# Performance work log

Hardware: AMD Instinct MI355X
Metric: run time of the kernel (lower is better)

The kernel has to match this reference:

```python
import jax, jax.numpy as jnp
import numpy as np

B, L, D = 16, 2048, 1024  # memory_len == input_len (mask is applied on both axes)
NEG = -1e20


def setup_inputs() -> dict:
    key = jax.random.key(0)
    k1, k2, k3, k4, k5, k6 = jax.random.split(key, 6)
    inp = jax.random.normal(k1, (B, L, D), dtype=jnp.float32)
    mem = jax.random.normal(k2, (B, L, D), dtype=jnp.float32)
    # True = masked-out position; keep sparsity low so rows stay mostly valid
    mask = jax.random.bernoulli(k3, 0.1, (B, L))
    inv = 1.0 / np.sqrt(D)
    w_input = jax.random.normal(k4, (D,), dtype=jnp.float32) * inv   # Linear(D,1) weight
    w_memory = jax.random.normal(k5, (D,), dtype=jnp.float32) * inv  # Linear(D,1) weight
    dot_scale = jax.random.uniform(k6, (D,), dtype=jnp.float32, minval=0.0, maxval=inv)
    return {"input": inp, "memory": mem, "mask": mask,
            "w_input": w_input, "w_memory": w_memory, "dot_scale": dot_scale}


def reference(input, memory, mask, w_input, w_memory, dot_scale):
    # dropout p = 0.0 -> identity
    input_dot = jnp.einsum("bld,d->bl", input, w_input)[:, :, None]   # [B,L,1]
    memory_dot = jnp.einsum("bmd,d->bm", memory, w_memory)[:, None, :]  # [B,1,M]
    cross_dot = jnp.einsum("bld,bmd->blm", input * dot_scale, memory)   # [B,L,M]
    att = input_dot + memory_dot + cross_dot
    bad = mask[:, :, None] | mask[:, None, :]                           # [B,L,M]
    att = jnp.where(bad, NEG, att)
    weight_one = jax.nn.softmax(att, axis=-1)                           # over memory axis
    output_one = jnp.einsum("blm,bmd->bld", weight_one, memory)
    weight_two = jax.nn.softmax(att.max(axis=-1), axis=-1)[:, None, :]  # [B,1,L]
    output_two = jnp.einsum("bol,bld->bod", weight_two, input)          # [B,1,D]
    return jnp.concatenate(
        [input, output_one, input * output_one, output_two * output_one], axis=-1)
```

## Files before the change

### kernel.cpp

```cpp
#include <hip/hip_runtime.h>
#include <hip/hip_bf16.h>


#define BDIM 16
#define LDIM 2048
#define MDIM 2048
#define DDIM 1024
#define NEGF (-60000.0f)

typedef float    f32x4v __attribute__((ext_vector_type(4)));
typedef _Float16 half8  __attribute__((ext_vector_type(8)));
typedef _Float16 half4  __attribute__((ext_vector_type(4)));

#define GL16(gp, lp)                                                        \
  __builtin_amdgcn_global_load_lds(                                         \
      (const __attribute__((address_space(1))) unsigned int*)(gp),          \
      (__attribute__((address_space(3))) unsigned int*)(lp), 16, 0, 0)

__device__ __forceinline__ float4 m4(const float4 a, const float4 b) {
  return (float4){a.x * b.x, a.y * b.y, a.z * b.z, a.w * b.w};
}
__device__ __forceinline__ void nts4(const float4 v, float* p) {
  f32x4v w = {v.x, v.y, v.z, v.w};
  __builtin_nontemporal_store(w, (f32x4v*)p);
}

__global__ __launch_bounds__(256) void conv_kernel(
    const float* __restrict__ input, const float* __restrict__ memory,
    const float* __restrict__ w_in, const float* __restrict__ w_mem,
    const float* __restrict__ scale,
    _Float16* __restrict__ Qh, _Float16* __restrict__ Kh,
    float* __restrict__ idot, float* __restrict__ mdot) {
  const int t = threadIdx.x, lane = t & 63, wid = t >> 6;
  const size_t row = (size_t)blockIdx.x * 4 + wid;
  const float* ir  = input  + row * DDIM;
  const float* mrp = memory + row * DDIM;
  float di = 0.f, dm = 0.f;
#pragma unroll
  for (int c = 0; c < 4; ++c) {
    const int off = c * 256 + lane * 4;
    float4 sc4 = *(const float4*)&scale[off];
    float4 wi4 = *(const float4*)&w_in[off];
    float4 wm4 = *(const float4*)&w_mem[off];
    float4 v = *(const float4*)&ir[off];
    di += v.x * wi4.x + v.y * wi4.y + v.z * wi4.z + v.w * wi4.w;
    half4 q = { (_Float16)(v.x * sc4.x), (_Float16)(v.y * sc4.y),
                (_Float16)(v.z * sc4.z), (_Float16)(v.w * sc4.w) };
    *(half4*)&Qh[row * DDIM + off] = q;
    float4 u = *(const float4*)&mrp[off];
    dm += u.x * wm4.x + u.y * wm4.y + u.z * wm4.z + u.w * wm4.w;
    half4 k = { (_Float16)u.x, (_Float16)u.y, (_Float16)u.z, (_Float16)u.w };
    *(half4*)&Kh[row * DDIM + off] = k;
  }
#pragma unroll
  for (int o = 1; o < 64; o <<= 1) {
    di += __shfl_xor(di, o, 64);
    dm += __shfl_xor(dm, o, 64);
  }
  if (lane == 0) { idot[row] = di; mdot[row] = dm; }
}

__global__ __launch_bounds__(256) void tr_kernel(const _Float16* __restrict__ Kh,
                                                 _Float16* __restrict__ Vt) {
  const int b = blockIdx.z;
  const int d0 = blockIdx.x * 64, m0 = blockIdx.y * 64;
  __shared__ _Float16 sT[64][80];
  const int t = threadIdx.x;
  {
    const int mr = t >> 2, ch = (t & 3) * 16;
    const _Float16* src = Kh + ((size_t)b * MDIM + m0 + mr) * DDIM + d0 + ch;
    *(half8*)&sT[mr][ch]     = *(const half8*)&src[0];
    *(half8*)&sT[mr][ch + 8] = *(const half8*)&src[8];
  }
  __syncthreads();
  {
    const int dr = t >> 2, mc = (t & 3) * 16;
    union { _Float16 h[16]; half8 v[2]; } tmp;
#pragma unroll
    for (int j = 0; j < 16; ++j) tmp.h[j] = sT[mc + j][dr];
    _Float16* dst = Vt + ((size_t)b * DDIM + d0 + dr) * MDIM + m0 + mc;
    *(half8*)&dst[0] = tmp.v[0];
    *(half8*)&dst[8] = tmp.v[1];
  }
}

__device__ __forceinline__ void stage128(const _Float16* __restrict__ Ab,
                                         const _Float16* __restrict__ Bb,
                                         _Float16* sAb, _Float16* sBb,
                                         int stride, int k0, int wid, int lane) {
  const int rsub = lane >> 3;
  const int sc = ((lane & 7) ^ rsub) * 8;
#pragma unroll
  for (int j = 0; j < 4; ++j) {
    const int r0 = wid * 32 + j * 8;
    const size_t go = (size_t)(r0 + rsub) * stride + k0 + sc;
    GL16(Ab + go, sAb + r0 * 64);
    GL16(Bb + go, sBb + r0 * 64);
  }
}

__device__ __forceinline__ void compute128(const _Float16* sAb, const _Float16* sBb,
                                           f32x4v acc[4][4], int wr, int wc,
                                           int lane) {
  const int l15 = lane & 15;
#pragma unroll
  for (int kk = 0; kk < 2; ++kk) {
    const int colh = ((kk * 4 + (lane >> 4)) ^ (lane & 7)) * 8;
    half8 aF[4], bF[4];
#pragma unroll
    for (int i = 0; i < 4; ++i) {
      aF[i] = *(const half8*)&sAb[(wr * 64 + i * 16 + l15) * 64 + colh];
      bF[i] = *(const half8*)&sBb[(wc * 64 + i * 16 + l15) * 64 + colh];
    }
#pragma unroll
    for (int mi = 0; mi < 4; ++mi)
#pragma unroll
      for (int ni = 0; ni < 4; ++ni)
        acc[mi][ni] = __builtin_amdgcn_mfma_f32_16x16x32_f16(aF[mi], bF[ni],
                                                             acc[mi][ni], 0, 0, 0);
  }
}

__global__ __launch_bounds__(256, 4) void gemm1_kernel(
    const _Float16* __restrict__ Qh, const _Float16* __restrict__ Kh,
    const float* __restrict__ idot, const float* __restrict__ mdot,
    const int* __restrict__ mask, _Float16* __restrict__ Sp) {
  const int id = blockIdx.x;
  const int wg = (id & 7) * 512 + (id >> 3);
  const int b = wg >> 8, rem = wg & 255, by = rem >> 4, bx = rem & 15;
  const int t = threadIdx.x, lane = t & 63, wid = t >> 6;
  const int wr = wid >> 1, wc = wid & 1;
  __shared__ union SM1 {
    struct { _Float16 a[128 * 64]; _Float16 b[128 * 64]; } ab;
    _Float16 s[128 * 140];
  } sm;
  __shared__ float s_dl[128], s_dm[128];
  __shared__ int   s_ml[128], s_mm[128];
  if (t < 128) {
    s_dl[t] = idot[b * LDIM + by * 128 + t];
    s_ml[t] = mask[b * LDIM + by * 128 + t];
    s_dm[t] = mdot[b * MDIM + bx * 128 + t];
    s_mm[t] = mask[b * MDIM + bx * 128 + t];
  }
  const _Float16* Ab = Qh + ((size_t)b * LDIM + by * 128) * DDIM;
  const _Float16* Bb = Kh + ((size_t)b * MDIM + bx * 128) * DDIM;
  f32x4v acc[4][4];
#pragma unroll
  for (int i = 0; i < 4; ++i)
#pragma unroll
    for (int j = 0; j < 4; ++j) acc[i][j] = (f32x4v){0.f, 0.f, 0.f, 0.f};

  for (int ks = 0; ks < DDIM / 64; ++ks) {
    __syncthreads();
    stage128(Ab, Bb, sm.ab.a, sm.ab.b, DDIM, ks * 64, wid, lane);
    __syncthreads();
    compute128(sm.ab.a, sm.ab.b, acc, wr, wc, lane);
  }

  __syncthreads();
  const int rb = wr * 64, cb = wc * 64;
#pragma unroll
  for (int mi = 0; mi < 4; ++mi)
#pragma unroll
    for (int ni = 0; ni < 4; ++ni)
#pragma unroll
      for (int r = 0; r < 4; ++r) {
        const int lrow = rb + mi * 16 + (lane >> 4) * 4 + r;
        const int lcol = cb + ni * 16 + (lane & 15);
        float s = acc[mi][ni][r] + s_dl[lrow] + s_dm[lcol];
        if ((s_ml[lrow] | s_mm[lcol]) != 0) s = NEGF;
        sm.s[lrow * 140 + lcol] = (_Float16)s;
      }
  __syncthreads();
  const int r16 = t >> 4, c8 = (t & 15) * 8;
#pragma unroll
  for (int rd = 0; rd < 8; ++rd) {
    const int lrow = rd * 16 + r16;
    half8 v = *(const half8*)&sm.s[lrow * 140 + c8];
    *(half8*)&Sp[((size_t)b * LDIM + by * 128 + lrow) * MDIM + bx * 128 + c8] = v;
  }
}

__global__ __launch_bounds__(256) void softmax_rows(_Float16* __restrict__ Sp,
                                                    float* __restrict__ rmax) {
  const int t = threadIdx.x, lane = t & 63, wid = t >> 6;
  const size_t row = (size_t)blockIdx.x * 4 + wid;
  _Float16* rp = Sp + row * (size_t)MDIM;
  float s[32];
#pragma unroll
  for (int c = 0; c < 4; ++c) {
    half8 v = *(const half8*)&rp[c * 512 + lane * 8];
#pragma unroll
    for (int j = 0; j < 8; ++j) s[c * 8 + j] = (float)v[j];
  }
  float m = -3.0e38f;
#pragma unroll
  for (int i = 0; i < 32; ++i) m = fmaxf(m, s[i]);
#pragma unroll
  for (int o = 1; o < 64; o <<= 1) m = fmaxf(m, __shfl_xor(m, o, 64));
  float sum = 0.f;
#pragma unroll
  for (int i = 0; i < 32; ++i) { s[i] = __expf(s[i] - m); sum += s[i]; }
#pragma unroll
  for (int o = 1; o < 64; o <<= 1) sum += __shfl_xor(sum, o, 64);
  const float inv = 1.f / sum;
#pragma unroll
  for (int c = 0; c < 4; ++c) {
    half8 v;
#pragma unroll
    for (int j = 0; j < 8; ++j) v[j] = (_Float16)(s[c * 8 + j] * inv);
    *(half8*)&rp[c * 512 + lane * 8] = v;
  }
  if (lane == 0) rmax[row] = m;
}

__global__ __launch_bounds__(256) void w2a_kernel(const float* __restrict__ rmax,
                                                  float* __restrict__ w2,
                                                  float* __restrict__ o2) {
  const int b = blockIdx.x, t = threadIdx.x;
  ((float4*)(o2 + (size_t)b * DDIM))[t] = (float4){0.f, 0.f, 0.f, 0.f};
  __shared__ float red[256];
  const float* rm = rmax + (size_t)b * LDIM;
  float vals[8]; float lm = -3.0e38f;
#pragma unroll
  for (int j = 0; j < 8; ++j) { vals[j] = rm[t + j * 256]; lm = fmaxf(lm, vals[j]); }
  red[t] = lm; __syncthreads();
  for (int s = 128; s > 0; s >>= 1) {
    if (t < s) red[t] = fmaxf(red[t], red[t + s]);
    __syncthreads();
  }
  const float M = red[0]; __syncthreads();
  float ls = 0.f;
#pragma unroll
  for (int j = 0; j < 8; ++j) ls += __expf(vals[j] - M);
  red[t] = ls; __syncthreads();
  for (int s = 128; s > 0; s >>= 1) {
    if (t < s) red[t] += red[t + s];
    __syncthreads();
  }
  const float inv = 1.f / red[0];
#pragma unroll
  for (int j = 0; j < 8; ++j) w2[(size_t)b * LDIM + t + j * 256] = __expf(vals[j] - M) * inv;
}

__global__ __launch_bounds__(256) void o2_kernel(const float* __restrict__ input,
                                                 const float* __restrict__ w2,
                                                 float* __restrict__ o2) {
  const int b = blockIdx.y, ch = blockIdx.x, t = threadIdx.x;
  __shared__ float sw[128];
  if (t < 128) sw[t] = w2[(size_t)b * LDIM + ch * 128 + t];
  __syncthreads();
  const float* ib = input + ((size_t)b * LDIM + ch * 128) * DDIM;
  float4 acc = {0.f, 0.f, 0.f, 0.f};
  for (int l = 0; l < 128; ++l) {
    const float w = sw[l];
    float4 v = *(const float4*)&ib[(size_t)l * DDIM + t * 4];
    acc.x += w * v.x; acc.y += w * v.y; acc.z += w * v.z; acc.w += w * v.w;
  }
  atomicAdd(&o2[b * DDIM + t * 4 + 0], acc.x);
  atomicAdd(&o2[b * DDIM + t * 4 + 1], acc.y);
  atomicAdd(&o2[b * DDIM + t * 4 + 2], acc.z);
  atomicAdd(&o2[b * DDIM + t * 4 + 3], acc.w);
}

__global__ __launch_bounds__(256, 4) void gemm2_kernel(
    const _Float16* __restrict__ Pm, const _Float16* __restrict__ Vt,
    const float* __restrict__ input, const float* __restrict__ o2,
    float* __restrict__ out) {
  const int id = blockIdx.x;
  const int wg = (id & 7) * 256 + (id >> 3);
  const int b = wg >> 7, rem = wg & 127, by = rem >> 3, bx = rem & 7;
  const int t = threadIdx.x, lane = t & 63, wid = t >> 6;
  const int wr = wid >> 1, wc = wid & 1;
  __shared__ union SM2 {
    struct { _Float16 a[128 * 64]; _Float16 b[128 * 64]; } ab;
    float c[16 * 132];
  } sm;
  const _Float16* Ab = Pm + ((size_t)b * LDIM + by * 128) * MDIM;
  const _Float16* Bb = Vt + ((size_t)b * DDIM + bx * 128) * MDIM;
  f32x4v acc[4][4];
#pragma unroll
  for (int i = 0; i < 4; ++i)
#pragma unroll
    for (int j = 0; j < 4; ++j) acc[i][j] = (f32x4v){0.f, 0.f, 0.f, 0.f};

  for (int ks = 0; ks < MDIM / 64; ++ks) {
    __syncthreads();
    stage128(Ab, Bb, sm.ab.a, sm.ab.b, MDIM, ks * 64, wid, lane);
    __syncthreads();
    compute128(sm.ab.a, sm.ab.b, acc, wr, wc, lane);
  }

  const int cq = (t & 15) * 4;
  const float4 o2a = *(const float4*)&o2[b * DDIM + bx * 128 + cq];
  const float4 o2b = *(const float4*)&o2[b * DDIM + bx * 128 + 64 + cq];
  const int r16 = t >> 4;
  __syncthreads();
#pragma unroll
  for (int pp = 0; pp < 8; ++pp) {
    if (wr == (pp >> 2)) {
      const int pmi = pp & 3;
#pragma unroll
      for (int ni = 0; ni < 4; ++ni)
#pragma unroll
        for (int r = 0; r < 4; ++r)
          sm.c[((lane >> 4) * 4 + r) * 132 + wc * 64 + ni * 16 + (lane & 15)] =
              acc[pmi][ni][r];
    }
    __syncthreads();
    const size_t l = (size_t)by * 128 + pp * 16 + r16;
    const float4 c0 = *(const float4*)&sm.c[r16 * 132 + cq];
    const float4 c1 = *(const float4*)&sm.c[r16 * 132 + 64 + cq];
    const float* ibp = &input[((size_t)b * LDIM + l) * DDIM + bx * 128];
    const float4 i0 = *(const float4*)&ibp[cq];
    const float4 i1 = *(const float4*)&ibp[64 + cq];
    float* ob = &out[((size_t)b * LDIM + l) * (4 * DDIM) + bx * 128];
    nts4(i0, ob + cq);
    nts4(i1, ob + 64 + cq);
    nts4(c0, ob + DDIM + cq);
    nts4(c1, ob + DDIM + 64 + cq);
    nts4(m4(i0, c0), ob + 2 * DDIM + cq);
    nts4(m4(i1, c1), ob + 2 * DDIM + 64 + cq);
    nts4(m4(o2a, c0), ob + 3 * DDIM + cq);
    nts4(m4(o2b, c1), ob + 3 * DDIM + 64 + cq);
    __syncthreads();
  }
}

extern "C" void kernel_launch(void* const* d_in, const int* in_sizes, int n_in,
                              void* d_out, int out_size, void* d_ws, size_t ws_size,
                              hipStream_t stream) {
  (void)in_sizes; (void)n_in; (void)out_size; (void)ws_size;
  const float* input  = (const float*)d_in[0];
  const float* memory = (const float*)d_in[1];
  const int*   mask   = (const int*)d_in[2];
  const float* w_in   = (const float*)d_in[3];
  const float* w_mem  = (const float*)d_in[4];
  const float* scale  = (const float*)d_in[5];
  float* out = (float*)d_out;

  char* p = (char*)d_ws;
  _Float16* Qh = (_Float16*)p; p += (size_t)BDIM * LDIM * DDIM * 2;
  _Float16* Kh = (_Float16*)p; p += (size_t)BDIM * MDIM * DDIM * 2;
  _Float16* Vt = (_Float16*)p; p += (size_t)BDIM * DDIM * MDIM * 2;
  _Float16* Sp = (_Float16*)p; p += (size_t)BDIM * LDIM * MDIM * 2;
  float* idot = (float*)p; p += (size_t)BDIM * LDIM * 4;
  float* mdot = (float*)p; p += (size_t)BDIM * MDIM * 4;
  float* rmax = (float*)p; p += (size_t)BDIM * LDIM * 4;
  float* w2   = (float*)p; p += (size_t)BDIM * LDIM * 4;
  float* o2   = (float*)p; p += (size_t)BDIM * DDIM * 4;

  conv_kernel<<<dim3(BDIM * LDIM / 4), dim3(256), 0, stream>>>(
      input, memory, w_in, w_mem, scale, Qh, Kh, idot, mdot);
  tr_kernel<<<dim3(DDIM / 64, MDIM / 64, BDIM), dim3(256), 0, stream>>>(Kh, Vt);
  gemm1_kernel<<<dim3(BDIM * 16 * 16), dim3(256), 0, stream>>>(
      Qh, Kh, idot, mdot, mask, Sp);
  softmax_rows<<<dim3(BDIM * LDIM / 4), dim3(256), 0, stream>>>(Sp, rmax);
  w2a_kernel<<<dim3(BDIM), dim3(256), 0, stream>>>(rmax, w2, o2);
  o2_kernel<<<dim3(LDIM / 128, BDIM), dim3(256), 0, stream>>>(input, w2, o2);
  gemm2_kernel<<<dim3(BDIM * 16 * 8), dim3(256), 0, stream>>>(
      Sp, Vt, input, o2, out);
}
```

Baseline: 552.9 us.

## Fuse memory conversion with V transpose and split input conversion kernel

The memory-side fp16 conversion, the w_mem dot product and the K→V transpose are merged into one kernel. It writes Kh and the transposed Vt straight from registers through shared memory, so the separate transpose pass no longer re-reads Kh. The input-side conversion becomes its own kernel. The o2 reduction also uses smaller chunks (32 rows instead of 128), giving 4x more blocks and more parallelism at the cost of more atomics. The fused memory kernel launches only 512 blocks and loops over 16 d-chunks with two barriers each, which may limit occupancy.

```diff
diff --git a/kernel.cpp b/kernel.cpp
--- a/kernel.cpp
+++ b/kernel.cpp
@@ -25,63 +25,79 @@
   __builtin_nontemporal_store(w, (f32x4v*)p);
 }
 
-__global__ __launch_bounds__(256) void conv_kernel(
-    const float* __restrict__ input, const float* __restrict__ memory,
-    const float* __restrict__ w_in, const float* __restrict__ w_mem,
-    const float* __restrict__ scale,
-    _Float16* __restrict__ Qh, _Float16* __restrict__ Kh,
-    float* __restrict__ idot, float* __restrict__ mdot) {
+__global__ __launch_bounds__(256) void conv_in(
+    const float* __restrict__ input, const float* __restrict__ w_in,
+    const float* __restrict__ scale, _Float16* __restrict__ Qh,
+    float* __restrict__ idot) {
   const int t = threadIdx.x, lane = t & 63, wid = t >> 6;
   const size_t row = (size_t)blockIdx.x * 4 + wid;
-  const float* ir  = input  + row * DDIM;
-  const float* mrp = memory + row * DDIM;
-  float di = 0.f, dm = 0.f;
+  const float* ir = input + row * DDIM;
+  float di = 0.f;
 #pragma unroll
   for (int c = 0; c < 4; ++c) {
     const int off = c * 256 + lane * 4;
     float4 sc4 = *(const float4*)&scale[off];
     float4 wi4 = *(const float4*)&w_in[off];
-    float4 wm4 = *(const float4*)&w_mem[off];
     float4 v = *(const float4*)&ir[off];
     di += v.x * wi4.x + v.y * wi4.y + v.z * wi4.z + v.w * wi4.w;
     half4 q = { (_Float16)(v.x * sc4.x), (_Float16)(v.y * sc4.y),
                 (_Float16)(v.z * sc4.z), (_Float16)(v.w * sc4.w) };
     *(half4*)&Qh[row * DDIM + off] = q;
-    float4 u = *(const float4*)&mrp[off];
-    dm += u.x * wm4.x + u.y * wm4.y + u.z * wm4.z + u.w * wm4.w;
-    half4 k = { (_Float16)u.x, (_Float16)u.y, (_Float16)u.z, (_Float16)u.w };
-    *(half4*)&Kh[row * DDIM + off] = k;
-  }
-#pragma unroll
-  for (int o = 1; o < 64; o <<= 1) {
-    di += __shfl_xor(di, o, 64);
-    dm += __shfl_xor(dm, o, 64);
-  }
-  if (lane == 0) { idot[row] = di; mdot[row] = dm; }
-}
-
-__global__ __launch_bounds__(256) void tr_kernel(const _Float16* __restrict__ Kh,
-                                                 _Float16* __restrict__ Vt) {
-  const int b = blockIdx.z;
-  const int d0 = blockIdx.x * 64, m0 = blockIdx.y * 64;
-  __shared__ _Float16 sT[64][80];
+  }
+#pragma unroll
+  for (int o = 1; o < 64; o <<= 1) di += __shfl_xor(di, o, 64);
+  if (lane == 0) idot[row] = di;
+}
+
+__global__ __launch_bounds__(256) void conv_mem(
+    const float* __restrict__ memory, const float* __restrict__ w_mem,
+    _Float16* __restrict__ Kh, _Float16* __restrict__ Vt,
+    float* __restrict__ mdot) {
+  const int b = blockIdx.y, m0 = blockIdx.x * 64;
   const int t = threadIdx.x;
-  {
-    const int mr = t >> 2, ch = (t & 3) * 16;
-    const _Float16* src = Kh + ((size_t)b * MDIM + m0 + mr) * DDIM + d0 + ch;
-    *(half8*)&sT[mr][ch]     = *(const half8*)&src[0];
-    *(half8*)&sT[mr][ch + 8] = *(const half8*)&src[8];
-  }
-  __syncthreads();
-  {
-    const int dr = t >> 2, mc = (t & 3) * 16;
-    union { _Float16 h[16]; half8 v[2]; } tmp;
-#pragma unroll
-    for (int j = 0; j < 16; ++j) tmp.h[j] = sT[mc + j][dr];
-    _Float16* dst = Vt + ((size_t)b * DDIM + d0 + dr) * MDIM + m0 + mc;
-    *(half8*)&dst[0] = tmp.v[0];
-    *(half8*)&dst[8] = tmp.v[1];
-  }
+  const int r = t >> 2, cs = (t & 3) * 16;
+  __shared__ _Float16 sT[64][66];
+  float dm = 0.f;
+  for (int ch = 0; ch < 16; ++ch) {
+    const int d0 = ch * 64;
+    const float* src = memory + ((size_t)b * MDIM + m0 + r) * DDIM + d0 + cs;
+    float4 v0 = *(const float4*)&src[0];
+    float4 v1 = *(const float4*)&src[4];
+    float4 v2 = *(const float4*)&src[8];
+    float4 v3 = *(const float4*)&src[12];
+    const float* wm = &w_mem[d0 + cs];
+    float4 w0 = *(const float4*)&wm[0];
+    float4 w1 = *(const float4*)&wm[4];
+    float4 w2v = *(const float4*)&wm[8];
+    float4 w3 = *(const float4*)&wm[12];
+    dm += v0.x * w0.x + v0.y * w0.y + v0.z * w0.z + v0.w * w0.w
+        + v1.x * w1.x + v1.y * w1.y + v1.z * w1.z + v1.w * w1.w
+        + v2.x * w2v.x + v2.y * w2v.y + v2.z * w2v.z + v2.w * w2v.w
+        + v3.x * w3.x + v3.y * w3.y + v3.z * w3.z + v3.w * w3.w;
+    half8 h0 = { (_Float16)v0.x, (_Float16)v0.y, (_Float16)v0.z, (_Float16)v0.w,
+                 (_Float16)v1.x, (_Float16)v1.y, (_Float16)v1.z, (_Float16)v1.w };
+    half8 h1 = { (_Float16)v2.x, (_Float16)v2.y, (_Float16)v2.z, (_Float16)v2.w,
+                 (_Float16)v3.x, (_Float16)v3.y, (_Float16)v3.z, (_Float16)v3.w };
+    _Float16* kp = &Kh[((size_t)b * MDIM + m0 + r) * DDIM + d0 + cs];
+    *(half8*)&kp[0] = h0;
+    *(half8*)&kp[8] = h1;
+    *(half8*)&sT[r][cs]     = h0;
+    *(half8*)&sT[r][cs + 8] = h1;
+    __syncthreads();
+    {
+      const int dr = r, ms = cs;
+      union { _Float16 h[16]; half8 v[2]; } tmp;
+#pragma unroll
+      for (int j = 0; j < 16; ++j) tmp.h[j] = sT[ms + j][dr];
+      _Float16* dst = Vt + ((size_t)b * DDIM + d0 + dr) * MDIM + m0 + ms;
+      *(half8*)&dst[0] = tmp.v[0];
+      *(half8*)&dst[8] = tmp.v[1];
+    }
+    __syncthreads();
+  }
+  dm += __shfl_xor(dm, 1);
+  dm += __shfl_xor(dm, 2);
+  if ((t & 3) == 0) mdot[(size_t)b * MDIM + m0 + r] = dm;
 }
 
 __device__ __forceinline__ void stage128(const _Float16* __restrict__ Ab,
@@ -247,12 +263,12 @@
                                                  const float* __restrict__ w2,
                                                  float* __restrict__ o2) {
   const int b = blockIdx.y, ch = blockIdx.x, t = threadIdx.x;
-  __shared__ float sw[128];
-  if (t < 128) sw[t] = w2[(size_t)b * LDIM + ch * 128 + t];
+  __shared__ float sw[32];
+  if (t < 32) sw[t] = w2[(size_t)b * LDIM + ch * 32 + t];
   __syncthreads();
-  const float* ib = input + ((size_t)b * LDIM + ch * 128) * DDIM;
+  const float* ib = input + ((size_t)b * LDIM + ch * 32) * DDIM;
   float4 acc = {0.f, 0.f, 0.f, 0.f};
-  for (int l = 0; l < 128; ++l) {
+  for (int l = 0; l < 32; ++l) {
     const float w = sw[l];
     float4 v = *(const float4*)&ib[(size_t)l * DDIM + t * 4];
     acc.x += w * v.x; acc.y += w * v.y; acc.z += w * v.z; acc.w += w * v.w;
@@ -350,14 +366,15 @@
   float* w2   = (float*)p; p += (size_t)BDIM * LDIM * 4;
   float* o2   = (float*)p; p += (size_t)BDIM * DDIM * 4;
 
-  conv_kernel<<<dim3(BDIM * LDIM / 4), dim3(256), 0, stream>>>(
-      input, memory, w_in, w_mem, scale, Qh, Kh, idot, mdot);
-  tr_kernel<<<dim3(DDIM / 64, MDIM / 64, BDIM), dim3(256), 0, stream>>>(Kh, Vt);
+  conv_in<<<dim3(BDIM * LDIM / 4), dim3(256), 0, stream>>>(
+      input, w_in, scale, Qh, idot);
+  conv_mem<<<dim3(MDIM / 64, BDIM), dim3(256), 0, stream>>>(
+      memory, w_mem, Kh, Vt, mdot);
   gemm1_kernel<<<dim3(BDIM * 16 * 16), dim3(256), 0, stream>>>(
       Qh, Kh, idot, mdot, mask, Sp);
   softmax_rows<<<dim3(BDIM * LDIM / 4), dim3(256), 0, stream>>>(Sp, rmax);
   w2a_kernel<<<dim3(BDIM), dim3(256), 0, stream>>>(rmax, w2, o2);
-  o2_kernel<<<dim3(LDIM / 128, BDIM), dim3(256), 0, stream>>>(input, w2, o2);
+  o2_kernel<<<dim3(LDIM / 32, BDIM), dim3(256), 0, stream>>>(input, w2, o2);
   gemm2_kernel<<<dim3(BDIM * 16 * 8), dim3(256), 0, stream>>>(
       Sp, Vt, input, o2, out);
 }
```

After: 560.3 us. Within noise of the previous version (+1.3%).
